# Kernel optimization log

Measured on AMD Instinct MI355X. Metric: run time of the kernel, lower is better.

Reference implementation:

```python
import jax, jax.numpy as jnp
import numpy as np

BATCH, IN_DIM, GRID, HID, DEPTH = 2048, 128, 128, 256, 7
BN_EPS = 1e-5


def setup_inputs() -> dict:
    key = jax.random.key(0)
    ks = jax.random.split(key, 10)
    x = jax.random.uniform(ks[0], (BATCH, IN_DIM), dtype=jnp.float32)
    grids = jax.random.uniform(ks[1], (DEPTH, IN_DIM, GRID), dtype=jnp.float32)  # torch.rand init
    fs = jax.random.normal(ks[2], (DEPTH, IN_DIM, GRID, HID), dtype=jnp.float32)
    depth_scores = jnp.ones((DEPTH,), dtype=jnp.float32)
    mlp_W = jax.random.normal(ks[3], (3, HID, HID), dtype=jnp.float32) * (1.0 / np.sqrt(HID))
    mlp_b = jnp.zeros((3, HID), dtype=jnp.float32)
    bn_gamma = jnp.ones((3, HID), dtype=jnp.float32)
    bn_beta = jnp.zeros((3, HID), dtype=jnp.float32)
    W_out = jax.random.normal(ks[4], (HID, 1), dtype=jnp.float32) * (1.0 / np.sqrt(HID))
    b_out = jnp.zeros((1,), dtype=jnp.float32)
    return {"x": x, "grids": grids, "fs": fs, "depth_scores": depth_scores,
            "mlp_W": mlp_W, "mlp_b": mlp_b, "bn_gamma": bn_gamma,
            "bn_beta": bn_beta, "W_out": W_out, "b_out": b_out}


def reference(x, grids, fs, depth_scores, mlp_W, mlp_b, bn_gamma, bn_beta, W_out, b_out):
    # per-feature min-max normalization over the batch dim
    xmin = x.min(axis=0, keepdims=True)
    xmax = x.max(axis=0, keepdims=True)
    z = (x - xmin) / (xmax - xmin + 1e-6)  # [B, I]

    outputs = []
    for i in range(DEPTH):
        Bmat = jax.nn.relu(z[:, :, None] - grids[i][None, :, :])  # [B, I, G]
        # (B.unsqueeze(-1) * fs[i]).sum(2).sum(1) == einsum big,igh->bh
        H = jnp.einsum('big,igh->bh', Bmat, fs[i])  # [B, H]
        if i > 0:  # residual accumulation
            H = H + outputs[-1]
        outputs.append(H)
    stacked = jnp.stack(outputs, axis=0)  # [D, B, H]
    w = jax.nn.softmax(depth_scores)  # depth attention
    h = jnp.einsum('d,dbh->bh', w, stacked)

    # MLP head (BatchNorm uses batch stats = training-mode behaviour; Dropout off)
    for j in range(3):
        h = h @ mlp_W[j] + mlp_b[j]
        mean = h.mean(axis=0)
        var = h.var(axis=0)  # biased, matching torch BN normalization
        h = (h - mean) * jax.lax.rsqrt(var + BN_EPS) * bn_gamma[j] + bn_beta[j]
        h = jax.nn.gelu(h, approximate=False)  # torch nn.GELU is exact erf GELU
    return h @ W_out + b_out
```

## Files before the change

kernel.cpp:

```cpp
#include <hip/hip_runtime.h>
#include <hip/hip_bf16.h>

#define BATCH 2048
#define IN_DIM 128
#define GRIDN 128
#define HID 256
#define DEPTH 7

typedef unsigned int u32;
typedef __attribute__((ext_vector_type(8))) short short8;
typedef __attribute__((ext_vector_type(4))) float floatx4;

#define OFF_FST   ((size_t)0)
#define SZ_FST    ((size_t)7*128*256*128*2)
#define OFF_ZT    (OFF_FST + SZ_FST)
#define SZ_ZT     ((size_t)BATCH*IN_DIM*4)
#define OFF_HPRE  (OFF_ZT + SZ_ZT)
#define SZ_HPRE   ((size_t)BATCH*HID*4)
#define OFF_STATS (OFF_HPRE + SZ_HPRE)
#define SZ_STATS  ((size_t)3*2*HID*4)
#define OFF_KEYS  (OFF_STATS + SZ_STATS)
#define SZ_KEYS   ((size_t)256*4)
#define OFF_CW    (OFF_KEYS + SZ_KEYS)
#define SZ_CW     ((size_t)32)
#define OFF_Y1    (OFF_CW + SZ_CW)
#define SZ_Y      ((size_t)BATCH*HID*4)
#define OFF_Y2    (OFF_Y1 + SZ_Y)
#define OFF_Y3    (OFF_Y2 + SZ_Y)

__device__ __forceinline__ void gload_lds16(const void* g, void* l) {
  __builtin_amdgcn_global_load_lds(
      (const __attribute__((address_space(1))) u32*)g,
      (__attribute__((address_space(3))) u32*)l, 16, 0, 0);
}

__device__ __forceinline__ u32 pack2_bf16(float lo, float hi) {
  __hip_bfloat162 b2;
  b2.x = __float2bfloat16(lo);
  b2.y = __float2bfloat16(hi);
  return *reinterpret_cast<u32*>(&b2);
}

__device__ __forceinline__ u32 pk_trunc(float a, float b) {
  return __builtin_amdgcn_perm(__float_as_uint(b), __float_as_uint(a), 0x07060302u);
}

__device__ __forceinline__ float reluc(float v) {
  return __builtin_amdgcn_fmed3f(v, 0.0f, 1.0f);
}

__device__ __forceinline__ float gelu_exact(float x) {
  return 0.5f * x * (1.0f + erff(x * 0.70710678118654752f));
}

__global__ void prep1_kernel(const float* __restrict__ x, u32* __restrict__ keys,
                             const float* __restrict__ depth_scores,
                             float* __restrict__ cw) {
  int t = threadIdx.x;
  int base = blockIdx.x * 256 + t;
  float mn = 1e30f, mx = -1e30f;
#pragma unroll
  for (int j = 0; j < 16; ++j) {
    float v = x[base + j * 16384];
    mn = fminf(mn, v); mx = fmaxf(mx, v);
  }
  __shared__ float smn[256], smx[256];
  smn[t] = mn; smx[t] = mx;
  __syncthreads();
  if (t < 128) {
    mn = fminf(smn[t], smn[t + 128]);
    mx = fmaxf(smx[t], smx[t + 128]);
    int i = base & 127;
    atomicMax(&keys[i], 0x7FFFFFFFu - __float_as_uint(mn));
    atomicMax(&keys[128 + i], __float_as_uint(mx));
  }
  if (blockIdx.x == 0 && t == 0) {
    float m = -1e30f;
    for (int d0 = 0; d0 < DEPTH; ++d0) m = fmaxf(m, depth_scores[d0]);
    float e[DEPTH]; float sum = 0.f;
    for (int d0 = 0; d0 < DEPTH; ++d0) { e[d0] = expf(depth_scores[d0] - m); sum += e[d0]; }
    float cacc = 0.f; float cs[DEPTH];
    for (int d0 = DEPTH - 1; d0 >= 0; --d0) { cacc += e[d0] / sum; cs[d0] = cacc; }
    for (int d0 = 0; d0 < DEPTH; ++d0) cw[d0] = cs[d0];
  }
}

__global__ void prep2_kernel(const float* __restrict__ x, const u32* __restrict__ keys,
                             float* __restrict__ z_t) {
  __shared__ float lds[128 * 65];
  int t = threadIdx.x;
  int b0 = blockIdx.x * 64;
#pragma unroll
  for (int q = 0; q < 32; ++q) {
    int idx = q * 256 + t;
    int b = idx >> 7, i = idx & 127;
    lds[i * 65 + b] = x[(size_t)(b0 + b) * IN_DIM + i];
  }
  __syncthreads();
#pragma unroll
  for (int q = 0; q < 32; ++q) {
    int idx = q * 256 + t;
    int ii = idx >> 6, bb = idx & 63;
    float mnv = __uint_as_float(0x7FFFFFFFu - keys[ii]);
    float mxv = __uint_as_float(keys[128 + ii]);
    float v = (lds[ii * 65 + bb] - mnv) * (1.0f / (mxv - mnv + 1e-6f));
    z_t[(size_t)ii * BATCH + b0 + bb] = v;
  }
}

__global__ void convert_kernel(const float* __restrict__ fs,
                               const float* __restrict__ cw,
                               __hip_bfloat16* __restrict__ fs2) {
  __shared__ u32 lds[256 * 33];
  int slab = blockIdx.x;
  int t = threadIdx.x;
  float cd = cw[slab >> 7];
  const float* src = fs + (size_t)slab * (GRIDN * HID);
  char* dstb = (char*)fs2 + (size_t)slab * 65536;

  for (int gh = 0; gh < 2; ++gh) {
    const float* s0 = src + (size_t)gh * 64 * HID + t;
#pragma unroll
    for (int g2 = 0; g2 < 32; ++g2) {
      float va = s0[(size_t)(2 * g2) * HID];
      float vb = s0[(size_t)(2 * g2 + 1) * HID];
      lds[t * 33 + g2] = pack2_bf16(cd * va, cd * vb);
    }
    __syncthreads();
#pragma unroll
    for (int it2 = 0; it2 < 8; ++it2) {
      int task = t + it2 * 256;
      int c = task >> 9;
      int q = task & 511;
      int nhalf = c >> 1, ksl = c & 1;
      int tt = q >> 6, l4 = (q >> 4) & 3, l15 = q & 15;
      int h = nhalf * 128 + tt * 16 + l15;
      int m = ksl * 4 + l4;
      u32 a0 = lds[h * 33 + m * 4 + 0];
      u32 a1 = lds[h * 33 + m * 4 + 1];
      u32 a2 = lds[h * 33 + m * 4 + 2];
      u32 a3 = lds[h * 33 + m * 4 + 3];
      size_t off = (size_t)nhalf * 32768 + (size_t)(gh * 2 + ksl) * 8192 +
                   (size_t)tt * 1024 + l4 * 256 + l15 * 16;
      *(uint4*)(dstb + off) = make_uint4(a0, a1, a2, a3);
    }
    __syncthreads();
  }
}

#define FENCE __asm__ volatile("" ::: "memory")
#define WAITV(c) do { __builtin_amdgcn_s_waitcnt(c); FENCE; } while (0)
#define BARR do { FENCE; __builtin_amdgcn_s_barrier(); FENCE; } while (0)
#define VM8 0x0F78
#define VM0 0x0F70

__launch_bounds__(256, 2)
__global__ void gemm_kernel(const float* __restrict__ z_t,
                            const float* __restrict__ grids,
                            const __hip_bfloat16* __restrict__ fs2,
                            float* __restrict__ h_pre) {
  __shared__ __align__(16) char lds[24576];

  int bx = blockIdx.x;
  int xcd = bx & 7;
  int t6 = bx >> 3;
  int cg = t6 >> 4;
  int jb2 = t6 & 15;
  int chunk = xcd + 8 * cg;
  int slab0 = chunk * 28;
  int mt = jb2 >> 1;
  int nh = jb2 & 1;

  int tid = threadIdx.x;
  int w = tid >> 6, l = tid & 63;
  int l15 = l & 15, l4 = l >> 4;
  int mbase = mt * 256 + w * 64;
  int nbase = nh * 128;

  floatx4 acc[4][8];
#pragma unroll
  for (int a = 0; a < 4; ++a)
#pragma unroll
    for (int b = 0; b < 8; ++b) acc[a][b] = (floatx4)0.f;

  const char* fsb = (const char*)fs2 + (size_t)slab0 * 65536 + (size_t)nh * 32768 +
                    (size_t)w * 2048 + (size_t)l * 16;

  auto stage8 = [&](int u, int bufIdx) {
    const char* srcb = fsb + (size_t)(u >> 2) * 65536 + (size_t)(u & 3) * 8192;
    char* dst = lds + bufIdx * 8192 + w * 2048;
    gload_lds16(srcb, dst);
    gload_lds16(srcb + 1024, dst + 1024);
  };

  float4 zA, zB;
  float4 g0A, g1A, g0B, g1B;
  auto zgload = [&](int s, float4& zv, float4& G0, float4& G1) {
    int slab = slab0 + (s >> 2);
    int iz = slab & 127;
    const float* zp = z_t + (size_t)iz * BATCH + mbase + l15;
    zv.x = zp[0]; zv.y = zp[16]; zv.z = zp[32]; zv.w = zp[48];
    const float* gp = grids + (size_t)slab * GRIDN + (s & 3) * 32 + l4 * 8;
    G0 = *(const float4*)gp;
    G1 = *(const float4*)(gp + 4);
  };

  short8 af[4];
  short8 bf[8];
  auto rdfrag8 = [&](int bufIdx) {
    const char* bp = lds + bufIdx * 8192 + l * 16;
#pragma unroll
    for (int tt = 0; tt < 8; ++tt)
      bf[tt] = *(const short8*)(bp + tt * 1024);
  };
  auto afgen = [&](const float4 zv, const float4 G0, const float4 G1) {
#pragma unroll
    for (int u = 0; u < 4; ++u) {
      float zu = (u == 0) ? zv.x : (u == 1) ? zv.y : (u == 2) ? zv.z : zv.w;
      union { uint4 q; short8 s8; } pk;
      pk.q.x = pk_trunc(reluc(zu - G0.x), reluc(zu - G0.y));
      pk.q.y = pk_trunc(reluc(zu - G0.z), reluc(zu - G0.w));
      pk.q.z = pk_trunc(reluc(zu - G1.x), reluc(zu - G1.y));
      pk.q.w = pk_trunc(reluc(zu - G1.z), reluc(zu - G1.w));
      af[u] = pk.s8;
    }
  };
  auto mfma32 = [&]() {
    __builtin_amdgcn_s_setprio(1);
#pragma unroll
    for (int u = 0; u < 4; ++u)
#pragma unroll
      for (int tt = 0; tt < 8; ++tt)
        acc[u][tt] = __builtin_amdgcn_mfma_f32_16x16x32_bf16(af[u], bf[tt], acc[u][tt], 0, 0, 0);
    __builtin_amdgcn_s_setprio(0);
  };

#define STEP_FULL(S, BUF, STBUF, ZV, G0, G1)                                   \
  do {                                                                         \
    WAITV(VM8); BARR;                                                          \
    stage8((S) + 2, (STBUF)); FENCE;                                           \
    rdfrag8(BUF);                                                              \
    afgen(ZV, G0, G1);                                                         \
    zgload((S) + 2, ZV, G0, G1); FENCE;                                        \
    mfma32();                                                                  \
  } while (0)

  stage8(0, 0); FENCE;
  zgload(0, zA, g0A, g1A); FENCE;
  stage8(1, 1); FENCE;
  zgload(1, zB, g0B, g1B); FENCE;

#pragma unroll 1
  for (int s0 = 0; s0 < 108; s0 += 6) {
    STEP_FULL(s0 + 0, 0, 2, zA, g0A, g1A);
    STEP_FULL(s0 + 1, 1, 0, zB, g0B, g1B);
    STEP_FULL(s0 + 2, 2, 1, zA, g0A, g1A);
    STEP_FULL(s0 + 3, 0, 2, zB, g0B, g1B);
    STEP_FULL(s0 + 4, 1, 0, zA, g0A, g1A);
    STEP_FULL(s0 + 5, 2, 1, zB, g0B, g1B);
  }

  STEP_FULL(108, 0, 2, zA, g0A, g1A);
  STEP_FULL(109, 1, 0, zB, g0B, g1B);
  WAITV(VM8); BARR;
  rdfrag8(2);
  afgen(zA, g0A, g1A);
  mfma32();
  WAITV(VM0); BARR;
  rdfrag8(0);
  afgen(zB, g0B, g1B);
  mfma32();

  int row0 = mbase + l4 * 4;
  int col0 = nbase + l15;
#pragma unroll
  for (int u = 0; u < 4; ++u) {
#pragma unroll
    for (int tt = 0; tt < 8; ++tt) {
      int col = col0 + tt * 16;
#pragma unroll
      for (int r = 0; r < 4; ++r) {
        int row = row0 + u * 16 + r;
        atomicAdd(&h_pre[(size_t)row * HID + col], acc[u][tt][r]);
      }
    }
  }
}

template <int FIRST>
__global__ void mlp_kernel(const float* __restrict__ Xin,
                           const float* __restrict__ statsIn,
                           const float* __restrict__ gamma,
                           const float* __restrict__ beta,
                           const float* __restrict__ W,
                           const float* __restrict__ bias,
                           float* __restrict__ Yout,
                           float* __restrict__ statsOut) {
  __shared__ float Xs[4][HID];
  int br = blockIdx.x, c = threadIdx.x;
  float mean = 0.f, rstd = 1.f, gm = 1.f, bt = 0.f;
  if (!FIRST) {
    float s1 = statsIn[c], s2 = statsIn[HID + c];
    mean = s1 * (1.0f / BATCH);
    float var = s2 * (1.0f / BATCH) - mean * mean;
    rstd = rsqrtf(var + 1e-5f);
    gm = gamma[c]; bt = beta[c];
  }
#pragma unroll
  for (int r = 0; r < 4; ++r) {
    float v = Xin[(size_t)(br * 4 + r) * HID + c];
    if (!FIRST) v = gelu_exact((v - mean) * rstd * gm + bt);
    Xs[r][c] = v;
  }
  __syncthreads();
  float acc[4] = {0, 0, 0, 0};
#pragma unroll 8
  for (int k = 0; k < HID; ++k) {
    float wv = W[(size_t)k * HID + c];
#pragma unroll
    for (int r = 0; r < 4; ++r) acc[r] += Xs[r][k] * wv;
  }
  float bb = bias[c];
  float s1 = 0.f, s2 = 0.f;
#pragma unroll
  for (int r = 0; r < 4; ++r) {
    float y = acc[r] + bb;
    Yout[(size_t)(br * 4 + r) * HID + c] = y;
    s1 += y; s2 += y * y;
  }
  atomicAdd(&statsOut[c], s1);
  atomicAdd(&statsOut[HID + c], s2);
}

__global__ void final_kernel(const float* __restrict__ Y3,
                             const float* __restrict__ statsIn,
                             const float* __restrict__ gamma,
                             const float* __restrict__ beta,
                             const float* __restrict__ W_out,
                             const float* __restrict__ b_out,
                             float* __restrict__ out) {
  int w = threadIdx.x >> 6, l = threadIdx.x & 63;
  int b = blockIdx.x * 4 + w;
  float4 y = *(const float4*)(Y3 + (size_t)b * HID + l * 4);
  float4 wv = *(const float4*)(W_out + l * 4);
  float r4[4] = {y.x, y.y, y.z, y.w};
  float w4[4] = {wv.x, wv.y, wv.z, wv.w};
  float s = 0.f;
  int c0 = l * 4;
#pragma unroll
  for (int q = 0; q < 4; ++q) {
    int c = c0 + q;
    float s1 = statsIn[c], s2 = statsIn[HID + c];
    float mean = s1 * (1.0f / BATCH);
    float var = s2 * (1.0f / BATCH) - mean * mean;
    float rstd = rsqrtf(var + 1e-5f);
    float v = gelu_exact((r4[q] - mean) * rstd * gamma[c] + beta[c]);
    s += v * w4[q];
  }
#pragma unroll
  for (int off = 32; off > 0; off >>= 1) s += __shfl_down(s, off);
  if (l == 0) out[b] = s + b_out[0];
}

extern "C" void kernel_launch(void* const* d_in, const int* in_sizes, int n_in,
                              void* d_out, int out_size, void* d_ws, size_t ws_size,
                              hipStream_t stream) {
  const float* x      = (const float*)d_in[0];
  const float* grids  = (const float*)d_in[1];
  const float* fs     = (const float*)d_in[2];
  const float* dscore = (const float*)d_in[3];
  const float* mlp_W  = (const float*)d_in[4];
  const float* mlp_b  = (const float*)d_in[5];
  const float* bn_g   = (const float*)d_in[6];
  const float* bn_b   = (const float*)d_in[7];
  const float* W_out  = (const float*)d_in[8];
  const float* b_out  = (const float*)d_in[9];
  float* out = (float*)d_out;

  char* ws = (char*)d_ws;
  __hip_bfloat16* fs2 = (__hip_bfloat16*)(ws + OFF_FST);
  float* z_t   = (float*)(ws + OFF_ZT);
  float* h_pre = (float*)(ws + OFF_HPRE);
  float* stats = (float*)(ws + OFF_STATS);
  u32*   keys  = (u32*)(ws + OFF_KEYS);
  float* cw    = (float*)(ws + OFF_CW);
  float* Y1    = (float*)(ws + OFF_Y1);
  float* Y2    = (float*)(ws + OFF_Y2);
  float* Y3    = (float*)(ws + OFF_Y3);

  hipMemsetAsync(h_pre, 0, SZ_HPRE + SZ_STATS + SZ_KEYS, stream);

  prep1_kernel<<<64, 256, 0, stream>>>(x, keys, dscore, cw);
  prep2_kernel<<<32, 256, 0, stream>>>(x, keys, z_t);
  convert_kernel<<<DEPTH * IN_DIM, 256, 0, stream>>>(fs, cw, fs2);
  gemm_kernel<<<512, 256, 0, stream>>>(z_t, grids, fs2, h_pre);

  mlp_kernel<1><<<512, 256, 0, stream>>>(h_pre, nullptr, nullptr, nullptr,
                                         mlp_W, mlp_b, Y1, stats);
  mlp_kernel<0><<<512, 256, 0, stream>>>(Y1, stats, bn_g, bn_b,
                                         mlp_W + 65536, mlp_b + 256, Y2, stats + 512);
  mlp_kernel<0><<<512, 256, 0, stream>>>(Y2, stats + 512, bn_g + 256, bn_b + 256,
                                         mlp_W + 2 * 65536, mlp_b + 2 * 256, Y3, stats + 1024);
  final_kernel<<<512, 256, 0, stream>>>(Y3, stats + 1024, bn_g + 512, bn_b + 512,
                                        W_out, b_out, out);
}
```

Before: 427.5 us.

## Fuse MLP head layers into one cooperative kernel with grid syncs

```diff
diff --git a/kernel.cpp b/kernel.cpp
--- a/kernel.cpp
+++ b/kernel.cpp
@@ -1,5 +1,8 @@
 #include <hip/hip_runtime.h>
 #include <hip/hip_bf16.h>
+#include <hip/hip_cooperative_groups.h>
+
+namespace cg = cooperative_groups;
 
 #define BATCH 2048
 #define IN_DIM 128
@@ -23,10 +26,6 @@
 #define SZ_KEYS   ((size_t)256*4)
 #define OFF_CW    (OFF_KEYS + SZ_KEYS)
 #define SZ_CW     ((size_t)32)
-#define OFF_Y1    (OFF_CW + SZ_CW)
-#define SZ_Y      ((size_t)BATCH*HID*4)
-#define OFF_Y2    (OFF_Y1 + SZ_Y)
-#define OFF_Y3    (OFF_Y2 + SZ_Y)
 
 __device__ __forceinline__ void gload_lds16(const void* g, void* l) {
   __builtin_amdgcn_global_load_lds(
@@ -164,9 +163,9 @@
   int bx = blockIdx.x;
   int xcd = bx & 7;
   int t6 = bx >> 3;
-  int cg = t6 >> 4;
+  int cg2 = t6 >> 4;
   int jb2 = t6 & 15;
-  int chunk = xcd + 8 * cg;
+  int chunk = xcd + 8 * cg2;
   int slab0 = chunk * 28;
   int mt = jb2 >> 1;
   int nh = jb2 & 1;
@@ -287,79 +286,64 @@
   }
 }
 
-template <int FIRST>
-__global__ void mlp_kernel(const float* __restrict__ Xin,
-                           const float* __restrict__ statsIn,
-                           const float* __restrict__ gamma,
-                           const float* __restrict__ beta,
-                           const float* __restrict__ W,
-                           const float* __restrict__ bias,
-                           float* __restrict__ Yout,
-                           float* __restrict__ statsOut) {
+__global__ void mlp_fused_kernel(const float* __restrict__ h_pre,
+                                 const float* __restrict__ mlp_W,
+                                 const float* __restrict__ mlp_b,
+                                 const float* __restrict__ bn_g,
+                                 const float* __restrict__ bn_b,
+                                 const float* __restrict__ W_out,
+                                 const float* __restrict__ b_out,
+                                 float* __restrict__ stats,
+                                 float* __restrict__ out) {
+  cg::grid_group grid = cg::this_grid();
   __shared__ float Xs[4][HID];
   int br = blockIdx.x, c = threadIdx.x;
-  float mean = 0.f, rstd = 1.f, gm = 1.f, bt = 0.f;
-  if (!FIRST) {
-    float s1 = statsIn[c], s2 = statsIn[HID + c];
-    mean = s1 * (1.0f / BATCH);
-    float var = s2 * (1.0f / BATCH) - mean * mean;
-    rstd = rsqrtf(var + 1e-5f);
-    gm = gamma[c]; bt = beta[c];
-  }
-#pragma unroll
-  for (int r = 0; r < 4; ++r) {
-    float v = Xin[(size_t)(br * 4 + r) * HID + c];
-    if (!FIRST) v = gelu_exact((v - mean) * rstd * gm + bt);
-    Xs[r][c] = v;
-  }
+
+#pragma unroll
+  for (int r = 0; r < 4; ++r)
+    Xs[r][c] = h_pre[(size_t)(br * 4 + r) * HID + c];
   __syncthreads();
-  float acc[4] = {0, 0, 0, 0};
+
+#pragma unroll 1
+  for (int j = 0; j < 3; ++j) {
+    const float* W = mlp_W + j * 65536;
+    float acc[4] = {0.f, 0.f, 0.f, 0.f};
 #pragma unroll 8
-  for (int k = 0; k < HID; ++k) {
-    float wv = W[(size_t)k * HID + c];
-#pragma unroll
-    for (int r = 0; r < 4; ++r) acc[r] += Xs[r][k] * wv;
-  }
-  float bb = bias[c];
-  float s1 = 0.f, s2 = 0.f;
-#pragma unroll
-  for (int r = 0; r < 4; ++r) {
-    float y = acc[r] + bb;
-    Yout[(size_t)(br * 4 + r) * HID + c] = y;
-    s1 += y; s2 += y * y;
-  }
-  atomicAdd(&statsOut[c], s1);
-  atomicAdd(&statsOut[HID + c], s2);
-}
-
-__global__ void final_kernel(const float* __restrict__ Y3,
-                             const float* __restrict__ statsIn,
-                             const float* __restrict__ gamma,
-                             const float* __restrict__ beta,
-                             const float* __restrict__ W_out,
-                             const float* __restrict__ b_out,
-                             float* __restrict__ out) {
-  int w = threadIdx.x >> 6, l = threadIdx.x & 63;
-  int b = blockIdx.x * 4 + w;
-  float4 y = *(const float4*)(Y3 + (size_t)b * HID + l * 4);
-  float4 wv = *(const float4*)(W_out + l * 4);
-  float r4[4] = {y.x, y.y, y.z, y.w};
-  float w4[4] = {wv.x, wv.y, wv.z, wv.w};
+    for (int k = 0; k < HID; ++k) {
+      float wv = W[(size_t)k * HID + c];
+#pragma unroll
+      for (int r = 0; r < 4; ++r) acc[r] += Xs[r][k] * wv;
+    }
+    float bb = mlp_b[j * 256 + c];
+    float y[4];
+    float s1 = 0.f, s2 = 0.f;
+#pragma unroll
+    for (int r = 0; r < 4; ++r) {
+      y[r] = acc[r] + bb;
+      s1 += y[r]; s2 += y[r] * y[r];
+    }
+    atomicAdd(&stats[j * 512 + c], s1);
+    atomicAdd(&stats[j * 512 + HID + c], s2);
+    __threadfence();
+    grid.sync();
+    float m = stats[j * 512 + c] * (1.0f / BATCH);
+    float var = stats[j * 512 + HID + c] * (1.0f / BATCH) - m * m;
+    float rstd = rsqrtf(var + 1e-5f);
+    float gm = bn_g[j * 256 + c], bt = bn_b[j * 256 + c];
+#pragma unroll
+    for (int r = 0; r < 4; ++r)
+      Xs[r][c] = gelu_exact((y[r] - m) * rstd * gm + bt);
+    __syncthreads();
+  }
+
+  int w = c >> 6, l = c & 63;
   float s = 0.f;
   int c0 = l * 4;
 #pragma unroll
-  for (int q = 0; q < 4; ++q) {
-    int c = c0 + q;
-    float s1 = statsIn[c], s2 = statsIn[HID + c];
-    float mean = s1 * (1.0f / BATCH);
-    float var = s2 * (1.0f / BATCH) - mean * mean;
-    float rstd = rsqrtf(var + 1e-5f);
-    float v = gelu_exact((r4[q] - mean) * rstd * gamma[c] + beta[c]);
-    s += v * w4[q];
-  }
+  for (int q = 0; q < 4; ++q) s += Xs[w][c0 + q] * W_out[c0 + q];
 #pragma unroll
   for (int off = 32; off > 0; off >>= 1) s += __shfl_down(s, off);
-  if (l == 0) out[b] = s + b_out[0];
+  if (l == 0) out[br * 4 + w] = s + b_out[0];
 }
 
 extern "C" void kernel_launch(void* const* d_in, const int* in_sizes, int n_in,
@@ -384,9 +368,6 @@
   float* stats = (float*)(ws + OFF_STATS);
   u32*   keys  = (u32*)(ws + OFF_KEYS);
   float* cw    = (float*)(ws + OFF_CW);
-  float* Y1    = (float*)(ws + OFF_Y1);
-  float* Y2    = (float*)(ws + OFF_Y2);
-  float* Y3    = (float*)(ws + OFF_Y3);
 
   hipMemsetAsync(h_pre, 0, SZ_HPRE + SZ_STATS + SZ_KEYS, stream);
 
@@ -395,12 +376,9 @@
   convert_kernel<<<DEPTH * IN_DIM, 256, 0, stream>>>(fs, cw, fs2);
   gemm_kernel<<<512, 256, 0, stream>>>(z_t, grids, fs2, h_pre);
 
-  mlp_kernel<1><<<512, 256, 0, stream>>>(h_pre, nullptr, nullptr, nullptr,
-                                         mlp_W, mlp_b, Y1, stats);
-  mlp_kernel<0><<<512, 256, 0, stream>>>(Y1, stats, bn_g, bn_b,
-                                         mlp_W + 65536, mlp_b + 256, Y2, stats + 512);
-  mlp_kernel<0><<<512, 256, 0, stream>>>(Y2, stats + 512, bn_g + 256, bn_b + 256,
-                                         mlp_W + 2 * 65536, mlp_b + 2 * 256, Y3, stats + 1024);
-  final_kernel<<<512, 256, 0, stream>>>(Y3, stats + 1024, bn_g + 512, bn_b + 512,
-                                        W_out, b_out, out);
-}
+  void* args[] = {(void*)&h_pre, (void*)&mlp_W, (void*)&mlp_b, (void*)&bn_g,
+                  (void*)&bn_b, (void*)&W_out, (void*)&b_out, (void*)&stats,
+                  (void*)&out};
+  hipLaunchCooperativeKernel((const void*)mlp_fused_kernel, dim3(512), dim3(256),
+                             args, 0, stream);
+}
```

Result: slower. 681.5 us (+59.4%).
